# Optimization experiments

Measured on AMD Instinct MI355X. Metric: run time of the kernel, lower is better.

## Reference

```python
import jax, jax.numpy as jnp
import numpy as np

H, D = 8, 128           # num_heads, head_dim
HID = 1024              # hidden_size
K = 4                   # short conv kernel
EPS_QK = 1e-6
EPS_NORM = 1e-5


def short_conv(x, w):
    # x: (B, T, C), w: (C, 1, K) depthwise causal conv (zero initial state) + SiLU
    k = w.shape[-1]
    xp = jnp.pad(x, ((0, 0), (k - 1, 0), (0, 0)))
    xc = jnp.transpose(xp, (0, 2, 1))  # (B, C, T+K-1)
    y = jax.lax.conv_general_dilated(xc, w, window_strides=(1,), padding='VALID',
                                     feature_group_count=w.shape[0])
    return jax.nn.silu(jnp.transpose(y, (0, 2, 1)))


def _rmsn(t, eps):
    return t * jax.lax.rsqrt(jnp.mean(t * t, axis=-1, keepdims=True) + eps)


def setup_inputs() -> dict:
    key = jax.random.key(0)
    ks = jax.random.split(key, 16)
    s = 0.02
    inp = {
        'x': jax.random.normal(ks[0], (2, 1024, HID), dtype=jnp.float32),
        'Wq': jax.random.normal(ks[1], (H * D, HID), dtype=jnp.float32) * s,
        'Wk': jax.random.normal(ks[2], (H * D, HID), dtype=jnp.float32) * s,
        'Wv': jax.random.normal(ks[3], (H * D, HID), dtype=jnp.float32) * s,
        'wq_conv': jax.random.normal(ks[4], (H * D, 1, K), dtype=jnp.float32) * 0.3,
        'wk_conv': jax.random.normal(ks[5], (H * D, 1, K), dtype=jnp.float32) * 0.3,
        'wv_conv': jax.random.normal(ks[6], (H * D, 1, K), dtype=jnp.float32) * 0.3,
        'Wfa': jax.random.normal(ks[7], (D, HID), dtype=jnp.float32) * s,
        'Wfb': jax.random.normal(ks[8], (H * D, D), dtype=jnp.float32) * s,
        'Wb': jax.random.normal(ks[9], (H, HID), dtype=jnp.float32) * s,
        'Wga': jax.random.normal(ks[10], (D, HID), dtype=jnp.float32) * s,
        'Wgb': jax.random.normal(ks[11], (H * D, D), dtype=jnp.float32) * s,
        'A_log': jnp.log(jax.random.uniform(ks[12], (H,), minval=1.0, maxval=16.0, dtype=jnp.float32)),
        'dt_bias': jnp.zeros((H, D), dtype=jnp.float32),
        'o_norm_w': jnp.ones((D,), dtype=jnp.float32),
        'Wo': jax.random.normal(ks[13], (HID, H * D), dtype=jnp.float32) * s,
    }
    return inp


def reference(x, Wq, Wk, Wv, wq_conv, wk_conv, wv_conv, Wfa, Wfb, Wb, Wga, Wgb,
              A_log, dt_bias, o_norm_w, Wo):
    B, T, _ = x.shape
    scale = float(D) ** -0.5

    q = short_conv(x @ Wq.T, wq_conv).reshape(B, T, H, D)
    k = short_conv(x @ Wk.T, wk_conv).reshape(B, T, H, D)
    v = short_conv(x @ Wv.T, wv_conv).reshape(B, T, H, D)

    q = (scale ** 2) * _rmsn(q, EPS_QK)
    k = scale * _rmsn(k, EPS_QK)

    a_logits = ((x @ Wfa.T) @ Wfb.T).reshape(B, T, H, D)
    g = -jnp.exp(A_log)[None, None, :, None] * jax.nn.softplus(a_logits + dt_bias)  # (B,T,H,D)
    beta = jax.nn.sigmoid(x @ Wb.T)  # (B,T,H)

    # gated delta-rule recurrence over time; state S: (B, H, Dk, Dv)
    def step(S, inputs):
        q_t, k_t, v_t, g_t, b_t = inputs
        S = S * jnp.exp(g_t)[..., None]                       # per-channel decay on key dim
        kv = jnp.einsum('bhd,bhdv->bhv', k_t, S)              # read
        delta = b_t[..., None] * (v_t - kv)                   # beta-gated delta
        S = S + k_t[..., None] * delta[:, :, None, :]         # rank-1 write
        o = jnp.einsum('bhd,bhdv->bhv', q_t, S)
        return S, o

    tb = lambda t: jnp.moveaxis(t, 1, 0)  # (B,T,...) -> (T,B,...)
    S0 = jnp.zeros((B, H, D, D), dtype=x.dtype)
    _, o_t = jax.lax.scan(step, S0, (tb(q), tb(k), tb(v), tb(g), tb(beta)))
    out = jnp.moveaxis(o_t, 0, 1)  # (B, T, H, D)

    gate = ((x @ Wga.T) @ Wgb.T).reshape(B, T, H, D)
    out = _rmsn(out, EPS_NORM) * o_norm_w * jax.nn.sigmoid(gate)
    return out.reshape(B, T, H * D) @ Wo.T
```

## Files before the change

### kernel.cpp

```cpp
#include <hip/hip_runtime.h>
#include <hip/hip_bf16.h>
#include <math.h>

#define H 8
#define D 128
#define HID 1024
#define KCONV 4

typedef __bf16 bhalf;
typedef __bf16 bhalf4 __attribute__((ext_vector_type(4)));
typedef __bf16 bhalf8 __attribute__((ext_vector_type(8)));
typedef float f32x4 __attribute__((ext_vector_type(4)));
typedef _Float16 hlf;
typedef _Float16 half8 __attribute__((ext_vector_type(8)));
typedef _Float16 half4v __attribute__((ext_vector_type(4)));

__device__ __forceinline__ void async16(const void* g, void* l) {
    __builtin_amdgcn_global_load_lds(
        (const __attribute__((address_space(1))) void*)g,
        (__attribute__((address_space(3))) void*)l, 16, 0, 0);
}

__global__ __launch_bounds__(256) void gemm_bf16_nt(const bhalf* A, const bhalf* B,
                                                    void* Cv,
                                                    int M, int N, int K,
                                                    int lda, int ldb, int ldc, int epi,
                                                    const float* __restrict__ A_log,
                                                    const float* __restrict__ dt_bias,
                                                    const bhalf* A2, const bhalf* B2,
                                                    void* C2, int epi2,
                                                    bhalf* __restrict__ pXAG,
                                                    float* __restrict__ pBETA)
{
    if (blockIdx.z) { A = A2; B = B2; Cv = C2; epi = epi2; }
    __shared__ __align__(16) bhalf As[128][32];
    __shared__ __align__(16) bhalf Bs[64][32];
    int tid = threadIdx.x;
    int wid = tid >> 6, lane = tid & 63;
    int rowBase = blockIdx.y * 128;
    int colBase = blockIdx.x * 64;
    int wm = wid >> 1, wn = wid & 1;

    f32x4 acc[4][2] = {};

    int r = lane >> 2;
    int cseg = lane & 3;

    for (int k0 = 0; k0 < K; k0 += 32) {
        __syncthreads();
#pragma unroll
        for (int s = 0; s < 3; ++s) {
            int j = wid * 3 + s;
            if (j < 8) {
                const bhalf* ga = A + (size_t)(rowBase + j * 16 + r) * lda + k0 + cseg * 8;
                async16(ga, &As[j * 16][0]);
            } else {
                int jb = j - 8;
                const bhalf* ga = B + (size_t)(colBase + jb * 16 + r) * ldb + k0 + cseg * 8;
                async16(ga, &Bs[jb * 16][0]);
            }
        }
        __syncthreads();
        int mq = lane & 15, kq = (lane >> 4) * 8;
        bhalf8 af[4], bfr[2];
#pragma unroll
        for (int mt = 0; mt < 4; ++mt)
            af[mt] = *(const bhalf8*)&As[wm * 64 + mt * 16 + mq][kq];
#pragma unroll
        for (int nt = 0; nt < 2; ++nt)
            bfr[nt] = *(const bhalf8*)&Bs[wn * 32 + nt * 16 + mq][kq];
#pragma unroll
        for (int mt = 0; mt < 4; ++mt)
#pragma unroll
            for (int nt = 0; nt < 2; ++nt)
                acc[mt][nt] = __builtin_amdgcn_mfma_f32_16x16x32_bf16(
                    af[mt], bfr[nt], acc[mt][nt], 0, 0, 0);
    }
    int rquad = (lane >> 4) * 4;
#pragma unroll
    for (int mt = 0; mt < 4; ++mt) {
        int m0 = rowBase + wm * 64 + mt * 16 + rquad;
#pragma unroll
        for (int nt = 0; nt < 2; ++nt) {
            int c = colBase + wn * 32 + (lane & 15) + nt * 16;
#pragma unroll
            for (int rr = 0; rr < 4; ++rr) {
                float val = acc[mt][nt][rr];
                int m = m0 + rr;
                if (epi == 0) {
                    ((float*)Cv)[(size_t)m * ldc + c] = val;
                } else if (epi == 1) {
                    int h = c >> 7, d = c & 127;
                    float z = val + dt_bias[h * D + d];
                    float sp = (z > 20.f) ? z : log1pf(expf(z));
                    ((float*)Cv)[(size_t)m * ldc + c] = expf(-expf(A_log[h]) * sp);
                } else if (epi == 2) {
                    ((bhalf*)Cv)[(size_t)m * ldc + c] = (bhalf)val;
                } else {
                    if (c < 3072) {
                        ((float*)Cv)[(size_t)m * 3072 + c] = val;
                    } else if (c < 3328) {
                        pXAG[(size_t)m * 256 + (c - 3072)] = (bhalf)val;
                    } else if (c < 3336) {
                        pBETA[(size_t)m * 8 + (c - 3328)] = 1.f / (1.f + expf(-val));
                    }
                }
            }
        }
    }
}

__global__ void cast1(const float* __restrict__ s, bhalf* __restrict__ d, int n4)
{
    int i = blockIdx.x * blockDim.x + threadIdx.x;
    if (i >= n4) return;
    float4 v = ((const float4*)s)[i];
    bhalf4 o = {(bhalf)v.x, (bhalf)v.y, (bhalf)v.z, (bhalf)v.w};
    ((bhalf4*)d)[i] = o;
}
__global__ void cast4(const float* __restrict__ s0, const float* __restrict__ s1,
                      const float* __restrict__ s2, const float* __restrict__ s3,
                      bhalf* __restrict__ d0, bhalf* __restrict__ d1,
                      bhalf* __restrict__ d2, bhalf* __restrict__ d3, int n4)
{
    int i = blockIdx.x * blockDim.x + threadIdx.x;
    if (i >= n4) return;
    int a = blockIdx.y;
    const float* s = (a == 0) ? s0 : (a == 1) ? s1 : (a == 2) ? s2 : s3;
    bhalf* d = (a == 0) ? d0 : (a == 1) ? d1 : (a == 2) ? d2 : d3;
    float4 v = ((const float4*)s)[i];
    bhalf4 o = {(bhalf)v.x, (bhalf)v.y, (bhalf)v.z, (bhalf)v.w};
    ((bhalf4*)d)[i] = o;
}

__global__ __launch_bounds__(128) void conv3_kernel(const float* __restrict__ QKV,
                                                    const float* __restrict__ wq,
                                                    const float* __restrict__ wk,
                                                    const float* __restrict__ wv,
                                                    float* __restrict__ Qc,
                                                    float* __restrict__ Kc,
                                                    float* __restrict__ Vc,
                                                    int T)
{
    int which = blockIdx.y;
    const float* w; float* out; int mode; float scale;
    if (which == 0)      { w = wq; out = Qc; mode = 1; scale = 1.0f / 128.0f; }
    else if (which == 1) { w = wk; out = Kc; mode = 1; scale = 0.08838834764831845f; }
    else                 { w = wv; out = Vc; mode = 0; scale = 1.f; }

    int bid = blockIdx.x;
    int h = bid % H;
    int t = (bid / H) % T;
    int b = bid / (H * T);
    int d = threadIdx.x;
    int c = h * D + d;
    const float* base = QKV + (size_t)b * T * 3072 + which * 1024 + c;
    float acc = 0.f;
#pragma unroll
    for (int j = 0; j < KCONV; ++j) {
        int tt = t - (KCONV - 1) + j;
        float xv = (tt >= 0) ? base[(size_t)tt * 3072] : 0.f;
        acc += xv * w[c * KCONV + j];
    }
    float y = acc / (1.f + expf(-acc));
    if (mode) {
        __shared__ float red[2];
        float ss = y * y;
#pragma unroll
        for (int s = 32; s > 0; s >>= 1) ss += __shfl_xor(ss, s, 64);
        if ((threadIdx.x & 63) == 0) red[threadIdx.x >> 6] = ss;
        __syncthreads();
        float tot = red[0] + red[1];
        float r = rsqrtf(tot * (1.f / D) + 1e-6f);
        y = y * r * scale;
    }
    out[(size_t)bid * D + d] = y;
}

template <int CTRL>
__device__ __forceinline__ float dpp_add(float x) {
    int y = __builtin_amdgcn_update_dpp(0, __builtin_bit_cast(int, x),
                                        CTRL, 0xF, 0xF, false);
    return x + __builtin_bit_cast(float, y);
}
__device__ __forceinline__ float wave_sum63(float x) {
    x = dpp_add<0x111>(x);
    x = dpp_add<0x112>(x);
    x = dpp_add<0x114>(x);
    x = dpp_add<0x118>(x);
    x = dpp_add<0x142>(x);
    x = dpp_add<0x143>(x);
    return x;
}


__global__ __launch_bounds__(256) void chunk_prep_kernel(
    const float* __restrict__ Q, const float* __restrict__ K,
    const float* __restrict__ V, const float* __restrict__ E,
    const float* __restrict__ BETA,
    hlf* __restrict__ Wn, float* __restrict__ Uf, hlf* __restrict__ Qt,
    hlf* __restrict__ AoL, hlf* __restrict__ KbT, float* __restrict__ Aend,
    int T)
{
    __shared__ __align__(16) float e_s[32][128];
    __shared__ __align__(16) float k_s[32][128];
    __shared__ __align__(16) float U_s[32][128];
    __shared__ __align__(16) hlf  A_s[32][128];
    __shared__ __align__(16) hlf  W_s[32][128];
    __shared__ float P_s[32][32];
    __shared__ float Ao_s[32][32];
    __shared__ float beta_s[32];

    int tid = threadIdx.x, wid = tid >> 6, lane = tid & 63;
    int bid = blockIdx.x;
    int bh = bid >> 5, ch = bid & 31;
    int b = bh >> 3, h = bh & 7;
    int t0 = ch * 32;
    size_t rowb = (size_t)(b * T + t0) * 1024 + h * 128;
    size_t co = (size_t)bh * 32 + ch;

    int rs2 = lane >> 5, seg = (lane & 31) * 4;
#pragma unroll
    for (int p = wid * 4; p < wid * 4 + 4; ++p) {
        int row = p * 2 + rs2;
        async16(E + rowb + (size_t)row * 1024 + seg, &e_s[p * 2][0]);
        async16(K + rowb + (size_t)row * 1024 + seg, &k_s[p * 2][0]);
    }
    __syncthreads();

    for (int x = tid; x < 1024; x += 256) Ao_s[x >> 5][x & 31] = 0.f;
    if (wid == 2 && lane < 32)
        beta_s[lane] = BETA[(size_t)(b * T + t0 + lane) * 8 + h];
    int d0 = lane * 2;
    if (wid == 0) {
        float a0 = 1.f, a1 = 1.f;
        for (int t = 0; t < 32; ++t) {
            a0 *= e_s[t][d0]; a1 *= e_s[t][d0 + 1];
            A_s[t][d0] = (hlf)a0; A_s[t][d0 + 1] = (hlf)a1;
        }
        Aend[co * 128 + d0] = a0; Aend[co * 128 + d0 + 1] = a1;
    } else if (wid == 1) {
        float s0 = 1.f, s1 = 1.f;
        for (int t = 31; t >= 0; --t) {
            KbT[co * 4096 + (size_t)d0 * 32 + t]       = (hlf)(k_s[t][d0] * s0);
            KbT[co * 4096 + (size_t)(d0 + 1) * 32 + t] = (hlf)(k_s[t][d0 + 1] * s1);
            s0 *= e_s[t][d0]; s1 *= e_s[t][d0 + 1];
        }
    }
    __syncthreads();

#pragma unroll
    for (int ii = 0; ii < 8; ++ii) {
        int i = wid + ii * 4;
        float ki0 = k_s[i][d0], ki1 = k_s[i][d0 + 1];
        float2 qv = *(const float2*)(Q + rowb + (size_t)i * 1024 + d0);
        float aa = wave_sum63(qv.x * ki0 + qv.y * ki1);
        if (lane == 63) Ao_s[i][i] = aa;
        float R0 = 1.f, R1 = 1.f;
        for (int j = i - 1; j >= 0; --j) {
            R0 *= e_s[j + 1][d0]; R1 *= e_s[j + 1][d0 + 1];
            float u0 = R0 * k_s[j][d0], u1 = R1 * k_s[j][d0 + 1];
            float pp = wave_sum63(ki0 * u0 + ki1 * u1);
            float a2 = wave_sum63(qv.x * u0 + qv.y * u1);
            if (lane == 63) { P_s[i][j] = pp; Ao_s[i][j] = a2; }
        }
    }
    __syncthreads();

    for (int x = tid; x < 1024; x += 256) {
        int i2 = x >> 5, j2 = x & 31;
        P_s[i2][j2] = (j2 < i2) ? P_s[i2][j2] * beta_s[i2] : 0.f;
    }
    __syncthreads();

    if (wid == 0) {
        for (int i = 0; i < 32; ++i) {
            float bb = beta_s[i];
            float a0 = bb * k_s[i][d0] * (float)A_s[i][d0];
            float a1 = bb * k_s[i][d0 + 1] * (float)A_s[i][d0 + 1];
            for (int k2 = 0; k2 < i; ++k2) {
                float L = P_s[i][k2];
                a0 -= L * (float)W_s[k2][d0];
                a1 -= L * (float)W_s[k2][d0 + 1];
            }
            W_s[i][d0] = (hlf)a0; W_s[i][d0 + 1] = (hlf)a1;
        }
    } else if (wid == 1) {
        for (int i = 0; i < 32; ++i) {
            float bb = beta_s[i];
            float2 vv = *(const float2*)(V + rowb + (size_t)i * 1024 + d0);
            float a0 = bb * vv.x, a1 = bb * vv.y;
            for (int k2 = 0; k2 < i; ++k2) {
                float L = P_s[i][k2];
                a0 -= L * U_s[k2][d0];
                a1 -= L * U_s[k2][d0 + 1];
            }
            U_s[i][d0] = a0; U_s[i][d0 + 1] = a1;
        }
    } else {
        for (int r2 = wid - 2; r2 < 32; r2 += 2) {
            float2 qv = *(const float2*)(Q + rowb + (size_t)r2 * 1024 + d0);
            Qt[co * 4096 + (size_t)r2 * 128 + d0]     = (hlf)(qv.x * (float)A_s[r2][d0]);
            Qt[co * 4096 + (size_t)r2 * 128 + d0 + 1] = (hlf)(qv.y * (float)A_s[r2][d0 + 1]);
        }
    }
    __syncthreads();

    for (int x = tid; x < 4096; x += 256) {
        Wn[co * 4096 + x] = (hlf)(-(float)W_s[x >> 7][x & 127]);
        Uf[co * 4096 + x] = U_s[x >> 7][x & 127];
    }
    for (int x = tid; x < 1024; x += 256)
        AoL[co * 1024 + x] = (hlf)Ao_s[x >> 5][x & 31];
}

struct ScanOps {
    half8 aw0, aw1, aw2, aw3;
    half8 aq0, aq1, aq2, aq3;
    half8 bK0, bK1, bK2, bK3;
    half8 aA;
    float u0, u1, u2, u3;
    f32x4 ae0, ae1, ae2, ae3;
};

__device__ __forceinline__ void scan_load(ScanOps& o, size_t co,
    const hlf* __restrict__ Wn, const float* __restrict__ Uf,
    const hlf* __restrict__ Qt, const hlf* __restrict__ Ao,
    const hlf* __restrict__ KbT, const float* __restrict__ Aend,
    int tr, int vc, int dseg, int mq, int kq, int rq, int v0)
{
    const hlf*   Wc  = Wn  + co * 4096;
    const hlf*   Qc  = Qt  + co * 4096;
    const hlf*   Aoc = Ao  + co * 1024;
    const hlf*   Kbc = KbT + co * 4096;
    const float* Uc  = Uf  + co * 4096;
    const float* Aec = Aend + co * 128;
    size_t rw = (size_t)(tr + mq) * 128 + kq;
    o.aw0 = *(const half8*)&Wc[rw];
    o.aw1 = *(const half8*)&Wc[rw + 32];
    o.aw2 = *(const half8*)&Wc[rw + 64];
    o.aw3 = *(const half8*)&Wc[rw + 96];
    o.aq0 = *(const half8*)&Qc[rw];
    o.aq1 = *(const half8*)&Qc[rw + 32];
    o.aq2 = *(const half8*)&Qc[rw + 64];
    o.aq3 = *(const half8*)&Qc[rw + 96];
    o.aA  = *(const half8*)&Aoc[(tr + mq) * 32 + kq];
    o.bK0 = *(const half8*)&Kbc[(size_t)(dseg + mq) * 32 + kq];
    o.bK1 = *(const half8*)&Kbc[(size_t)(dseg + 16 + mq) * 32 + kq];
    o.bK2 = *(const half8*)&Kbc[(size_t)(dseg + 32 + mq) * 32 + kq];
    o.bK3 = *(const half8*)&Kbc[(size_t)(dseg + 48 + mq) * 32 + kq];
    size_t ru = (size_t)(tr + rq) * 128 + v0 + vc + mq;
    o.u0 = Uc[ru];
    o.u1 = Uc[ru + 128];
    o.u2 = Uc[ru + 256];
    o.u3 = Uc[ru + 384];
    o.ae0 = *(const f32x4*)&Aec[dseg + rq];
    o.ae1 = *(const f32x4*)&Aec[dseg + 16 + rq];
    o.ae2 = *(const f32x4*)&Aec[dseg + 32 + rq];
    o.ae3 = *(const f32x4*)&Aec[dseg + 48 + rq];
}

__device__ __forceinline__ void scan_body(const ScanOps& o, int c,
    f32x4* sreg, hlf (*Sh)[136], hlf (*Dt)[40], float* __restrict__ O,
    int b, int h, int v0s, int T, int Mrows,
    int tr, int vc, int vtile, int dseg, int mq, int kq, int rq)
{
    half8 bs0 = *(const half8*)&Sh[vc + mq][kq];
    half8 bs1 = *(const half8*)&Sh[vc + mq][32 + kq];
    half8 bs2 = *(const half8*)&Sh[vc + mq][64 + kq];
    half8 bs3 = *(const half8*)&Sh[vc + mq][96 + kq];

    f32x4 dacc = {o.u0, o.u1, o.u2, o.u3};
    dacc = __builtin_amdgcn_mfma_f32_16x16x32_f16(o.aw0, bs0, dacc, 0, 0, 0);
    dacc = __builtin_amdgcn_mfma_f32_16x16x32_f16(o.aw1, bs1, dacc, 0, 0, 0);
    dacc = __builtin_amdgcn_mfma_f32_16x16x32_f16(o.aw2, bs2, dacc, 0, 0, 0);
    dacc = __builtin_amdgcn_mfma_f32_16x16x32_f16(o.aw3, bs3, dacc, 0, 0, 0);
    half4v dh4 = {(hlf)dacc[0], (hlf)dacc[1], (hlf)dacc[2], (hlf)dacc[3]};
    *(half4v*)&Dt[vc + mq][tr + rq] = dh4;

    asm volatile("s_waitcnt lgkmcnt(0)" ::: "memory");
    __builtin_amdgcn_s_barrier();
    __builtin_amdgcn_sched_barrier(0);

    f32x4 oacc = {0.f, 0.f, 0.f, 0.f};
    oacc = __builtin_amdgcn_mfma_f32_16x16x32_f16(o.aq0, bs0, oacc, 0, 0, 0);
    oacc = __builtin_amdgcn_mfma_f32_16x16x32_f16(o.aq1, bs1, oacc, 0, 0, 0);
    oacc = __builtin_amdgcn_mfma_f32_16x16x32_f16(o.aq2, bs2, oacc, 0, 0, 0);
    oacc = __builtin_amdgcn_mfma_f32_16x16x32_f16(o.aq3, bs3, oacc, 0, 0, 0);
    half8 bD = *(const half8*)&Dt[vc + mq][kq];
    oacc = __builtin_amdgcn_mfma_f32_16x16x32_f16(o.aA, bD, oacc, 0, 0, 0);
    size_t ob = (size_t)v0s * Mrows * 256 +
                ((size_t)(b * T + c * 32 + tr + rq) * 8 + h) * 32 + vc + mq;
    O[ob]       = oacc[0];
    O[ob + 256] = oacc[1];
    O[ob + 512] = oacc[2];
    O[ob + 768] = oacc[3];

    half8 aD = *(const half8*)&Dt[vtile + mq][kq];
    f32x4 s0 = sreg[0] * o.ae0;
    f32x4 s1 = sreg[1] * o.ae1;
    f32x4 s2 = sreg[2] * o.ae2;
    f32x4 s3 = sreg[3] * o.ae3;
    s0 = __builtin_amdgcn_mfma_f32_16x16x32_f16(o.bK0, aD, s0, 0, 0, 0);
    s1 = __builtin_amdgcn_mfma_f32_16x16x32_f16(o.bK1, aD, s1, 0, 0, 0);
    s2 = __builtin_amdgcn_mfma_f32_16x16x32_f16(o.bK2, aD, s2, 0, 0, 0);
    s3 = __builtin_amdgcn_mfma_f32_16x16x32_f16(o.bK3, aD, s3, 0, 0, 0);
    sreg[0] = s0; sreg[1] = s1; sreg[2] = s2; sreg[3] = s3;
    {
        half4v h0 = {(hlf)s0[0], (hlf)s0[1], (hlf)s0[2], (hlf)s0[3]};
        half4v h1 = {(hlf)s1[0], (hlf)s1[1], (hlf)s1[2], (hlf)s1[3]};
        half4v h2 = {(hlf)s2[0], (hlf)s2[1], (hlf)s2[2], (hlf)s2[3]};
        half4v h3 = {(hlf)s3[0], (hlf)s3[1], (hlf)s3[2], (hlf)s3[3]};
        *(half4v*)&Sh[vtile + mq][dseg + rq]      = h0;
        *(half4v*)&Sh[vtile + mq][dseg + 16 + rq] = h1;
        *(half4v*)&Sh[vtile + mq][dseg + 32 + rq] = h2;
        *(half4v*)&Sh[vtile + mq][dseg + 48 + rq] = h3;
    }
    asm volatile("s_waitcnt lgkmcnt(0)" ::: "memory");
    __builtin_amdgcn_s_barrier();
    __builtin_amdgcn_sched_barrier(0);
}

__global__ __launch_bounds__(256, 1) void chunk_scan_kernel(
    const hlf* __restrict__ Wn, const float* __restrict__ Uf,
    const hlf* __restrict__ Qt, const hlf* __restrict__ Ao,
    const hlf* __restrict__ KbT, const float* __restrict__ Aend,
    float* __restrict__ O, int T)
{
    __shared__ __align__(16) hlf  Sh[32][136];
    __shared__ __align__(16) hlf  Dt[32][40];

    int tid = threadIdx.x, wid = tid >> 6, lane = tid & 63;
    int nbh = gridDim.x >> 2;
    int bh = blockIdx.x % nbh, vs = blockIdx.x / nbh;
    int b = bh >> 3, h = bh & 7;
    int v0 = vs * 32;
    int Mrows = (nbh >> 3) * T;

    for (int x = tid; x < 32 * 136; x += 256) ((hlf*)Sh)[x] = (hlf)0.f;

    int mq = lane & 15, kq = (lane >> 4) * 8, rq = (lane >> 4) * 4;
    int tr = (wid >> 1) * 16, vc = (wid & 1) * 16;
    int vtile = (wid >> 1) * 16, dseg = (wid & 1) * 64;

    f32x4 sreg[4] = {};

    int NC = T / 32;
    size_t cb = (size_t)bh * 32;
    ScanOps opA, opB;
    scan_load(opA, cb, Wn, Uf, Qt, Ao, KbT, Aend, tr, vc, dseg, mq, kq, rq, v0);
    __syncthreads();

    for (int cc = 0; cc < NC; cc += 2) {
        scan_load(opB, cb + cc + 1, Wn, Uf, Qt, Ao, KbT, Aend,
                  tr, vc, dseg, mq, kq, rq, v0);
        scan_body(opA, cc, sreg, Sh, Dt, O, b, h, vs, T, Mrows,
                  tr, vc, vtile, dseg, mq, kq, rq);
        if (cc + 2 < NC)
            scan_load(opA, cb + cc + 2, Wn, Uf, Qt, Ao, KbT, Aend,
                      tr, vc, dseg, mq, kq, rq, v0);
        scan_body(opB, cc + 1, sreg, Sh, Dt, O, b, h, vs, T, Mrows,
                  tr, vc, vtile, dseg, mq, kq, rq);
    }
}

__global__ __launch_bounds__(128) void outnorm_kernel(const float* __restrict__ O,
                                                      const float* __restrict__ GATE,
                                                      const float* __restrict__ w,
                                                      bhalf* __restrict__ Obf,
                                                      int Mrows)
{
    int bid = blockIdx.x;
    int d = threadIdx.x;
    size_t base = (size_t)bid * D;
    float y = O[(size_t)(d >> 5) * Mrows * 256 + (size_t)bid * 32 + (d & 31)];
    __shared__ float red[2];
    float ss = y * y;
#pragma unroll
    for (int s = 32; s > 0; s >>= 1) ss += __shfl_xor(ss, s, 64);
    if ((threadIdx.x & 63) == 0) red[threadIdx.x >> 6] = ss;
    __syncthreads();
    float tot = red[0] + red[1];
    float r = rsqrtf(tot * (1.f / D) + 1e-5f);
    float gz = GATE[base + d];
    float sg = 1.f / (1.f + expf(-gz));
    Obf[base + d] = (bhalf)(y * r * w[d] * sg);
}

extern "C" void kernel_launch(void* const* d_in, const int* in_sizes, int n_in,
                              void* d_out, int out_size, void* d_ws, size_t ws_size,
                              hipStream_t stream)
{
    const float* x       = (const float*)d_in[0];
    const float* Wq      = (const float*)d_in[1];
    const float* Wk      = (const float*)d_in[2];
    const float* Wv      = (const float*)d_in[3];
    const float* wq_conv = (const float*)d_in[4];
    const float* wk_conv = (const float*)d_in[5];
    const float* wv_conv = (const float*)d_in[6];
    const float* Wfa     = (const float*)d_in[7];
    const float* Wfb     = (const float*)d_in[8];
    const float* Wb      = (const float*)d_in[9];
    const float* Wga     = (const float*)d_in[10];
    const float* Wgb     = (const float*)d_in[11];
    const float* A_log   = (const float*)d_in[12];
    const float* dt_bias = (const float*)d_in[13];
    const float* o_norm_w= (const float*)d_in[14];
    const float* Wo      = (const float*)d_in[15];

    int BT = in_sizes[0] / HID;
    int T = 1024;
    int B_ = BT / T;
    size_t M = (size_t)BT;
    size_t sz_big = M * HID;
    const int nW = HID * HID;
    const int nS = D * HID;
    const int NCAT = 3392;

    float* fp = (float*)d_ws;
    float* QKVp = fp;               fp += 3 * sz_big;
    float* Qc   = fp;               fp += sz_big;
    float* Kc   = fp;               fp += sz_big;
    float* Vc   = fp;               fp += sz_big;
    float* EGb  = fp;               fp += sz_big;
    float* GATE = fp;               fp += sz_big;
    float* Obuf = fp;               fp += sz_big;
    float* BETA = fp;               fp += M * H;
    bhalf* bp = (bhalf*)fp;
    bhalf* xb   = bp;               bp += sz_big;
    bhalf* Wcat = bp;               bp += (size_t)NCAT * HID;
    bhalf* Wob  = bp;               bp += nW;
    bhalf* Wfbb = bp;               bp += nS;
    bhalf* Wgbb = bp;               bp += nS;
    bhalf* XAG  = bp;               bp += M * 256;
    bhalf* Obf  = bp;               bp += sz_big;

    dim3 blk(256);

    cast1<<<(int)((sz_big / 4 + 255) / 256), 256, 0, stream>>>(x, xb, (int)(sz_big / 4));
    cast4<<<dim3((nW / 4 + 255) / 256, 4), 256, 0, stream>>>(Wq, Wk, Wv, Wo,
        Wcat, Wcat + nW, Wcat + 2 * (size_t)nW, Wob, nW / 4);
    cast4<<<dim3((nS / 4 + 255) / 256, 4), 256, 0, stream>>>(Wfa, Wga, Wfb, Wgb,
        Wcat + 3 * (size_t)nW, Wcat + 3 * (size_t)nW + nS, Wfbb, Wgbb, nS / 4);
    cast1<<<(H * HID / 4 + 255) / 256, 256, 0, stream>>>(Wb,
        Wcat + 3 * (size_t)nW + 2 * (size_t)nS, H * HID / 4);

    gemm_bf16_nt<<<dim3(NCAT / 64, BT / 128), blk, 0, stream>>>(
        xb, Wcat, QKVp, BT, NCAT, HID, HID, HID, 3072, 3, nullptr, nullptr,
        nullptr, nullptr, nullptr, 0, XAG, BETA);

    conv3_kernel<<<dim3(BT * H, 3), 128, 0, stream>>>(QKVp,
                                                      wq_conv, wk_conv, wv_conv,
                                                      Qc, Kc, Vc, T);

    gemm_bf16_nt<<<dim3(HID / 64, BT / 128, 2), blk, 0, stream>>>(
        XAG, Wfbb, EGb, BT, HID, D, 256, D, HID, 1, A_log, dt_bias,
        XAG + D, Wgbb, GATE, 0, nullptr, nullptr);

    int nbh = B_ * 8;
    float* Uf   = QKVp;
    float* Aend = Uf + (size_t)nbh * 32 * 4096;
    hlf* Wn  = (hlf*)(Aend + (size_t)nbh * 32 * 128);
    hlf* Qt  = Wn  + (size_t)nbh * 32 * 4096;
    hlf* AoLp= Qt  + (size_t)nbh * 32 * 4096;
    hlf* KbT = AoLp + (size_t)nbh * 32 * 1024;

    chunk_prep_kernel<<<nbh * 32, 256, 0, stream>>>(Qc, Kc, Vc, EGb, BETA,
                                                    Wn, Uf, Qt, AoLp, KbT, Aend, T);
    chunk_scan_kernel<<<nbh * 4, 256, 0, stream>>>(Wn, Uf, Qt, AoLp, KbT, Aend,
                                                   Obuf, T);

    outnorm_kernel<<<BT * H, 128, 0, stream>>>(Obuf, GATE, o_norm_w, Obf, BT);

    gemm_bf16_nt<<<dim3(HID / 64, BT / 128), blk, 0, stream>>>(
        Obf, Wob, (float*)d_out, BT, HID, HID, HID, HID, HID, 0, nullptr, nullptr,
        nullptr, nullptr, nullptr, 0, nullptr, nullptr);
}
```

Measured before the change: 319.8 us.

## Hand-schedule scan operand prefetch with inline asm loads and partial vmcnt waits

The chunked delta-rule scan now issues its per-chunk operand loads through inline-asm global loads and keeps two chunks in flight. Each body waits with s_waitcnt vmcnt(21), so only the older chunk's 21 loads must finish before it runs. The last chunk index is clamped so loads stay in bounds without a branch, and the explicit __syncthreads is replaced by an lgkmcnt wait plus a raw barrier. The chunk-prep kernel also stages V tiles into shared memory with async loads instead of reading global memory inside its serial loop. The hand-counted waits are fragile: other vector memory ops in the body, such as the O stores, could make the count incorrect.

Result: faster. 309.5 us, median of 2 (-3.2%).

```diff
diff --git a/kernel.cpp b/kernel.cpp
--- a/kernel.cpp
+++ b/kernel.cpp
@@ -225,6 +225,7 @@
         int row = p * 2 + rs2;
         async16(E + rowb + (size_t)row * 1024 + seg, &e_s[p * 2][0]);
         async16(K + rowb + (size_t)row * 1024 + seg, &k_s[p * 2][0]);
+        async16(V + rowb + (size_t)row * 1024 + seg, &U_s[p * 2][0]);
     }
     __syncthreads();
 
@@ -288,7 +289,7 @@
     } else if (wid == 1) {
         for (int i = 0; i < 32; ++i) {
             float bb = beta_s[i];
-            float2 vv = *(const float2*)(V + rowb + (size_t)i * 1024 + d0);
+            float2 vv = *(const float2*)&U_s[i][d0];
             float a0 = bb * vv.x, a1 = bb * vv.y;
             for (int k2 = 0; k2 < i; ++k2) {
                 float L = P_s[i][k2];
@@ -323,6 +324,20 @@
     f32x4 ae0, ae1, ae2, ae3;
 };
 
+#define GLOAD16(dst, ptr) \
+    asm volatile("global_load_dwordx4 %0, %1, off" : "=v"(dst) : "v"(ptr))
+#define GLOAD4(dst, ptr) \
+    asm volatile("global_load_dword %0, %1, off" : "=v"(dst) : "v"(ptr))
+
+#define SCAN_WAIT21(o) \
+    asm volatile("s_waitcnt vmcnt(21)" \
+        : "+v"(o.aw0), "+v"(o.aw1), "+v"(o.aw2), "+v"(o.aw3), \
+          "+v"(o.aq0), "+v"(o.aq1), "+v"(o.aq2), "+v"(o.aq3), \
+          "+v"(o.aA), \
+          "+v"(o.bK0), "+v"(o.bK1), "+v"(o.bK2), "+v"(o.bK3), \
+          "+v"(o.u0), "+v"(o.u1), "+v"(o.u2), "+v"(o.u3), \
+          "+v"(o.ae0), "+v"(o.ae1), "+v"(o.ae2), "+v"(o.ae3))
+
 __device__ __forceinline__ void scan_load(ScanOps& o, size_t co,
     const hlf* __restrict__ Wn, const float* __restrict__ Uf,
     const hlf* __restrict__ Qt, const hlf* __restrict__ Ao,
@@ -336,28 +351,28 @@
     const float* Uc  = Uf  + co * 4096;
     const float* Aec = Aend + co * 128;
     size_t rw = (size_t)(tr + mq) * 128 + kq;
-    o.aw0 = *(const half8*)&Wc[rw];
-    o.aw1 = *(const half8*)&Wc[rw + 32];
-    o.aw2 = *(const half8*)&Wc[rw + 64];
-    o.aw3 = *(const half8*)&Wc[rw + 96];
-    o.aq0 = *(const half8*)&Qc[rw];
-    o.aq1 = *(const half8*)&Qc[rw + 32];
-    o.aq2 = *(const half8*)&Qc[rw + 64];
-    o.aq3 = *(const half8*)&Qc[rw + 96];
-    o.aA  = *(const half8*)&Aoc[(tr + mq) * 32 + kq];
-    o.bK0 = *(const half8*)&Kbc[(size_t)(dseg + mq) * 32 + kq];
-    o.bK1 = *(const half8*)&Kbc[(size_t)(dseg + 16 + mq) * 32 + kq];
-    o.bK2 = *(const half8*)&Kbc[(size_t)(dseg + 32 + mq) * 32 + kq];
-    o.bK3 = *(const half8*)&Kbc[(size_t)(dseg + 48 + mq) * 32 + kq];
+    GLOAD16(o.aw0, &Wc[rw]);
+    GLOAD16(o.aw1, &Wc[rw + 32]);
+    GLOAD16(o.aw2, &Wc[rw + 64]);
+    GLOAD16(o.aw3, &Wc[rw + 96]);
+    GLOAD16(o.aq0, &Qc[rw]);
+    GLOAD16(o.aq1, &Qc[rw + 32]);
+    GLOAD16(o.aq2, &Qc[rw + 64]);
+    GLOAD16(o.aq3, &Qc[rw + 96]);
+    GLOAD16(o.aA,  &Aoc[(tr + mq) * 32 + kq]);
+    GLOAD16(o.bK0, &Kbc[(size_t)(dseg + mq) * 32 + kq]);
+    GLOAD16(o.bK1, &Kbc[(size_t)(dseg + 16 + mq) * 32 + kq]);
+    GLOAD16(o.bK2, &Kbc[(size_t)(dseg + 32 + mq) * 32 + kq]);
+    GLOAD16(o.bK3, &Kbc[(size_t)(dseg + 48 + mq) * 32 + kq]);
     size_t ru = (size_t)(tr + rq) * 128 + v0 + vc + mq;
-    o.u0 = Uc[ru];
-    o.u1 = Uc[ru + 128];
-    o.u2 = Uc[ru + 256];
-    o.u3 = Uc[ru + 384];
-    o.ae0 = *(const f32x4*)&Aec[dseg + rq];
-    o.ae1 = *(const f32x4*)&Aec[dseg + 16 + rq];
-    o.ae2 = *(const f32x4*)&Aec[dseg + 32 + rq];
-    o.ae3 = *(const f32x4*)&Aec[dseg + 48 + rq];
+    GLOAD4(o.u0, &Uc[ru]);
+    GLOAD4(o.u1, &Uc[ru + 128]);
+    GLOAD4(o.u2, &Uc[ru + 256]);
+    GLOAD4(o.u3, &Uc[ru + 384]);
+    GLOAD16(o.ae0, &Aec[dseg + rq]);
+    GLOAD16(o.ae1, &Aec[dseg + 16 + rq]);
+    GLOAD16(o.ae2, &Aec[dseg + 32 + rq]);
+    GLOAD16(o.ae3, &Aec[dseg + 48 + rq]);
 }
 
 __device__ __forceinline__ void scan_body(const ScanOps& o, int c,
@@ -447,21 +462,30 @@
 
     int NC = T / 32;
     size_t cb = (size_t)bh * 32;
-    ScanOps opA, opB;
-    scan_load(opA, cb, Wn, Uf, Qt, Ao, KbT, Aend, tr, vc, dseg, mq, kq, rq, v0);
-    __syncthreads();
-
+    size_t comax = (size_t)nbh * 32 - 1;
+
+    asm volatile("s_waitcnt lgkmcnt(0)" ::: "memory");
+    __builtin_amdgcn_s_barrier();
+
+    ScanOps op0, op1;
+    scan_load(op0, cb,     Wn, Uf, Qt, Ao, KbT, Aend, tr, vc, dseg, mq, kq, rq, v0);
+    scan_load(op1, cb + 1, Wn, Uf, Qt, Ao, KbT, Aend, tr, vc, dseg, mq, kq, rq, v0);
+
+#define CCLAMP(x) ((x) > comax ? comax : (x))
     for (int cc = 0; cc < NC; cc += 2) {
-        scan_load(opB, cb + cc + 1, Wn, Uf, Qt, Ao, KbT, Aend,
+        SCAN_WAIT21(op0);
+        scan_body(op0, cc, sreg, Sh, Dt, O, b, h, vs, T, Mrows,
+                  tr, vc, vtile, dseg, mq, kq, rq);
+        scan_load(op0, CCLAMP(cb + cc + 2), Wn, Uf, Qt, Ao, KbT, Aend,
                   tr, vc, dseg, mq, kq, rq, v0);
-        scan_body(opA, cc, sreg, Sh, Dt, O, b, h, vs, T, Mrows,
+
+        SCAN_WAIT21(op1);
+        scan_body(op1, cc + 1, sreg, Sh, Dt, O, b, h, vs, T, Mrows,
                   tr, vc, vtile, dseg, mq, kq, rq);
-        if (cc + 2 < NC)
-            scan_load(opA, cb + cc + 2, Wn, Uf, Qt, Ao, KbT, Aend,
-                      tr, vc, dseg, mq, kq, rq, v0);
-        scan_body(opB, cc + 1, sreg, Sh, Dt, O, b, h, vs, T, Mrows,
-                  tr, vc, vtile, dseg, mq, kq, rq);
-    }
+        scan_load(op1, CCLAMP(cb + cc + 3), Wn, Uf, Qt, Ao, KbT, Aend,
+                  tr, vc, dseg, mq, kq, rq, v0);
+    }
+#undef CCLAMP
 }
 
 __global__ __launch_bounds__(128) void outnorm_kernel(const float* __restrict__ O,
```
